# Kernel optimization log

Hardware: AMD Instinct MI355X
Metric: run time of the kernel (lower is better)

The kernel has to match this reference:

```python
import jax, jax.numpy as jnp
import numpy as np

N = 100000
E = 1600000
IN_CH, HID_CH, OUT_CH, HEADS = 128, 32, 64, 4
NEG_SLOPE = 0.2


def gat_conv(x, src, dst, W, att_src, att_dst, bias, concat):
    """PyG-style GATConv (inference; dropout off). src/dst include self-loops.
    x: [N, Fin], W: [Fin, H*C], att_*: [H, C], bias: [H*C] or [C]."""
    n = x.shape[0]
    H, C = att_src.shape
    h = (x @ W).reshape(n, H, C)                      # [N, H, C]
    a_s = jnp.sum(h * att_src, axis=-1)               # [N, H]
    a_d = jnp.sum(h * att_dst, axis=-1)               # [N, H]
    e = jax.nn.leaky_relu(a_s[src] + a_d[dst], NEG_SLOPE)   # [E, H]
    # segment softmax over incoming edges of each dst node
    e_max = jax.ops.segment_max(e, dst, num_segments=n)     # [N, H]
    e_exp = jnp.exp(e - e_max[dst])                          # [E, H]
    denom = jax.ops.segment_sum(e_exp, dst, num_segments=n) # [N, H]
    alpha = e_exp / (denom[dst] + 1e-16)                     # [E, H]
    msg = h[src] * alpha[:, :, None]                         # [E, H, C]
    out = jax.ops.segment_sum(msg, dst, num_segments=n)     # [N, H, C]
    out = out.reshape(n, H * C) if concat else out.mean(axis=1)
    return out + bias


def setup_inputs() -> dict:
    key = jax.random.key(0)
    ks = jax.random.split(key, 10)
    g = 1.0 / np.sqrt(IN_CH)
    g2 = 1.0 / np.sqrt(HID_CH * HEADS)
    return {
        "x": jax.random.normal(ks[0], (N, IN_CH), dtype=jnp.float32),
        "edge_index": jax.random.randint(ks[1], (2, E), 0, N, dtype=jnp.int64),
        "W1": jax.random.normal(ks[2], (IN_CH, HEADS * HID_CH), dtype=jnp.float32) * g,
        "att_src1": jax.random.normal(ks[3], (HEADS, HID_CH), dtype=jnp.float32) * g,
        "att_dst1": jax.random.normal(ks[4], (HEADS, HID_CH), dtype=jnp.float32) * g,
        "b1": jnp.zeros((HEADS * HID_CH,), dtype=jnp.float32),
        "W2": jax.random.normal(ks[5], (HEADS * HID_CH, OUT_CH), dtype=jnp.float32) * g2,
        "att_src2": jax.random.normal(ks[6], (1, OUT_CH), dtype=jnp.float32) * g2,
        "att_dst2": jax.random.normal(ks[7], (1, OUT_CH), dtype=jnp.float32) * g2,
        "b2": jnp.zeros((OUT_CH,), dtype=jnp.float32),
    }


def reference(x, edge_index, W1, att_src1, att_dst1, b1, W2, att_src2, att_dst2, b2):
    n = x.shape[0]
    # GATConv adds self-loops by default (fixed-size concat: jit friendly)
    loops = jnp.arange(n, dtype=edge_index.dtype)
    src = jnp.concatenate([edge_index[0], loops])
    dst = jnp.concatenate([edge_index[1], loops])
    h = gat_conv(x, src, dst, W1, att_src1, att_dst1, b1, concat=True)
    h = jax.nn.elu(h)
    return gat_conv(h, src, dst, W2, att_src2, att_dst2, b2, concat=False)
```

## Files before the change

kernel.cpp:

```cpp
#include <hip/hip_runtime.h>
#include <hip/hip_fp16.h>

#define NEG_SLOPE 0.2f
#define BKN 128
#define MAXNB 1024
#define GRP 256
#define LOG2E 1.44269504f

typedef _Float16 half_t;
typedef __attribute__((ext_vector_type(2))) _Float16 half2v;
typedef __attribute__((ext_vector_type(4))) _Float16 half4;
typedef __attribute__((ext_vector_type(8))) _Float16 half8;
typedef __attribute__((ext_vector_type(4))) float floatx4;

#if __has_builtin(__builtin_amdgcn_fdot2)
#define FDOT2(a, b, c) __builtin_amdgcn_fdot2((a), (b), (c), false)
#else
#define FDOT2(a, b, c) ((float)(a)[0] * (float)(b)[0] + (float)(a)[1] * (float)(b)[1] + (c))
#endif

template<int BN, int HEADS, bool INHALF>
__global__ __launch_bounds__(256) void gemm_mfma(
    const void* __restrict__ Xv, const half_t* __restrict__ Wt,
    const float* __restrict__ atts, const float* __restrict__ attd,
    half_t* __restrict__ H, float* __restrict__ As, float* __restrict__ Ad,
    int n)
{
    constexpr int K  = 128;
    constexpr int NT = BN / 16;
    constexpr int TPH = NT / HEADS;

    __shared__ half_t Wl[BN * K];
    __shared__ half_t Xl[64 * K];

    const int t = threadIdx.x;
    const int wave = t >> 6, lane = t & 63;
    const int quad = lane >> 4, c = lane & 15;

    float att_s[NT], att_d[NT];
    #pragma unroll
    for (int nt = 0; nt < NT; ++nt) {
        att_s[nt] = atts[nt * 16 + c] * LOG2E;
        att_d[nt] = attd[nt * 16 + c] * LOG2E;
    }

    for (int i = t; i < BN * 16; i += 256) {
        int row = i >> 4, cid = i & 15;
        half8 v = *(const half8*)(Wt + row * K + cid * 8);
        *(half8*)(Wl + row * K + ((cid ^ (row & 15)) << 3)) = v;
    }

    const int numTiles = (n + 63) / 64;
    for (int tile = blockIdx.x; tile < numTiles; tile += gridDim.x) {
        const int row0 = tile * 64;
        __syncthreads();
        for (int i = t; i < 1024; i += 256) {
            int m = i >> 4, cid = i & 15;
            int row = row0 + m;
            half8 h;
            #pragma unroll
            for (int z = 0; z < 8; ++z) h[z] = (half_t)0.f;
            if (row < n) {
                if constexpr (INHALF) {
                    h = *(const half8*)((const half_t*)Xv + (size_t)row * K + cid * 8);
                } else {
                    const float4* src = (const float4*)((const float*)Xv + (size_t)row * K + cid * 8);
                    float4 a = src[0], b = src[1];
                    h[0]=(half_t)a.x; h[1]=(half_t)a.y; h[2]=(half_t)a.z; h[3]=(half_t)a.w;
                    h[4]=(half_t)b.x; h[5]=(half_t)b.y; h[6]=(half_t)b.z; h[7]=(half_t)b.w;
                }
            }
            *(half8*)(Xl + m * K + ((cid ^ (m & 15)) << 3)) = h;
        }
        __syncthreads();

        floatx4 acc[NT];
        #pragma unroll
        for (int i = 0; i < NT; ++i) acc[i] = (floatx4)(0.f);

        #pragma unroll
        for (int kc = 0; kc < 4; ++kc) {
            int cid = kc * 4 + quad;
            half8 afrag = *(const half8*)(Xl + (wave * 16 + c) * K + ((cid ^ c) << 3));
            #pragma unroll
            for (int nt = 0; nt < NT; ++nt) {
                half8 bfrag = *(const half8*)(Wl + (nt * 16 + c) * K + ((cid ^ c) << 3));
                acc[nt] = __builtin_amdgcn_mfma_f32_16x16x32_f16(afrag, bfrag, acc[nt], 0, 0, 0);
            }
        }

        #pragma unroll
        for (int reg = 0; reg < 4; ++reg) {
            int row = row0 + wave * 16 + quad * 4 + reg;
            bool ok = row < n;
            if (ok) {
                #pragma unroll
                for (int nt = 0; nt < NT; ++nt)
                    H[(size_t)row * BN + nt * 16 + c] = (half_t)acc[nt][reg];
            }
            #pragma unroll
            for (int h = 0; h < HEADS; ++h) {
                float ps = 0.f, pd = 0.f;
                #pragma unroll
                for (int u = 0; u < TPH; ++u) {
                    int nt = h * TPH + u;
                    ps += acc[nt][reg] * att_s[nt];
                    pd += acc[nt][reg] * att_d[nt];
                }
                #pragma unroll
                for (int off = 1; off < 16; off <<= 1) {
                    ps += __shfl_xor(ps, off);
                    pd += __shfl_xor(pd, off);
                }
                if (ok && c == 0) {
                    As[(size_t)row * HEADS + h] = ps;
                    Ad[(size_t)row * HEADS + h] = pd;
                }
            }
        }
    }
}

__global__ __launch_bounds__(256) void ghist_wconv(
    const int* __restrict__ ei, int E, int Etot, int NB, int chunk,
    int* __restrict__ cnt,
    const float* __restrict__ W1, half_t* __restrict__ Wt1,
    const float* __restrict__ W2, half_t* __restrict__ Wt2)
{
    int iw = blockIdx.x * 256 + threadIdx.x;
    if (iw < 128 * 128) {
        int k = iw / 128, nn = iw % 128;
        Wt1[nn * 128 + k] = (half_t)W1[iw];
    } else if (iw < 128 * 128 + 128 * 64) {
        int jx = iw - 128 * 128;
        int k = jx / 64, nn = jx % 64;
        Wt2[nn * 128 + k] = (half_t)W2[jx];
    }

    __shared__ int h[MAXNB];
    int g = blockIdx.x;
    for (int i = threadIdx.x; i < NB; i += 256) h[i] = 0;
    __syncthreads();
    int lo = g * chunk, hi = min(Etot, lo + chunk);
    for (int e = lo + threadIdx.x; e < hi; e += 256) {
        int dst = (e < E) ? ei[E + e] : (e - E);
        atomicAdd(&h[dst >> 7], 1);
    }
    __syncthreads();
    for (int i = threadIdx.x; i < NB; i += 256) cnt[i * GRP + g] = h[i];
}

__global__ __launch_bounds__(256) void scan_blocks(
    int* __restrict__ data, int n, int* __restrict__ bsum)
{
    __shared__ int s[256];
    int t = threadIdx.x;
    int idx = blockIdx.x * 1024 + t * 4;
    int4 v = make_int4(0, 0, 0, 0);
    if (idx + 3 < n)      v = *(const int4*)(data + idx);
    else {
        if (idx     < n) v.x = data[idx];
        if (idx + 1 < n) v.y = data[idx+1];
        if (idx + 2 < n) v.z = data[idx+2];
        if (idx + 3 < n) v.w = data[idx+3];
    }
    int tsum = v.x + v.y + v.z + v.w;
    s[t] = tsum;
    __syncthreads();
    for (int off = 1; off < 256; off <<= 1) {
        int x = (t >= off) ? s[t - off] : 0;
        __syncthreads();
        s[t] += x;
        __syncthreads();
    }
    int excl = s[t] - tsum;
    if (t == 255) bsum[blockIdx.x] = s[255];
    if (idx     < n) data[idx]     = excl;
    if (idx + 1 < n) data[idx + 1] = excl + v.x;
    if (idx + 2 < n) data[idx + 2] = excl + v.x + v.y;
    if (idx + 3 < n) data[idx + 3] = excl + v.x + v.y + v.z;
}

__global__ __launch_bounds__(256) void scan_sums(int* __restrict__ bsum, int nb)
{
    __shared__ int s[256];
    int t = threadIdx.x;
    int v = (t < nb) ? bsum[t] : 0;
    s[t] = v;
    __syncthreads();
    for (int off = 1; off < 256; off <<= 1) {
        int x = (t >= off) ? s[t - off] : 0;
        __syncthreads();
        s[t] += x;
        __syncthreads();
    }
    if (t < nb) bsum[t] = s[t] - v;
}

__global__ __launch_bounds__(256) void pass1_gemm1(
    const int* __restrict__ ei, int E, int Etot, int NB, int chunk,
    const int* __restrict__ S, const int* __restrict__ bsum,
    unsigned* __restrict__ tmp,
    const float* __restrict__ X, const half_t* __restrict__ Wt,
    const float* __restrict__ atts, const float* __restrict__ attd,
    half_t* __restrict__ H, float* __restrict__ As, float* __restrict__ Ad,
    int n)
{
    constexpr int K = 128, BN = 128, NT = 8, HEADS = 4, TPH = 2;
    __shared__ half_t Wl[BN * K];
    __shared__ half_t Xl[64 * K];
    __shared__ int cur[MAXNB];

    const int t = threadIdx.x;

    if (blockIdx.x < GRP) {
        int g = blockIdx.x;
        for (int i = t; i < NB; i += 256) {
            int idx = i * GRP + g;
            cur[i] = S[idx] + bsum[idx >> 10];
        }
        __syncthreads();
        int lo = g * chunk, hi = min(Etot, lo + chunk);
        for (int e = lo + t; e < hi; e += 256) {
            int src, dst;
            if (e < E) { src = ei[e]; dst = ei[E + e]; }
            else       { src = dst = e - E; }
            int pos = atomicAdd(&cur[dst >> 7], 1);
            tmp[pos] = ((unsigned)src << 7) | (unsigned)(dst & (BKN - 1));
        }
        return;
    }

    const int wave = t >> 6, lane = t & 63;
    const int quad = lane >> 4, c = lane & 15;

    float att_s[NT], att_d[NT];
    #pragma unroll
    for (int nt = 0; nt < NT; ++nt) {
        att_s[nt] = atts[nt * 16 + c] * LOG2E;
        att_d[nt] = attd[nt * 16 + c] * LOG2E;
    }

    for (int i = t; i < BN * 16; i += 256) {
        int row = i >> 4, cid = i & 15;
        half8 v = *(const half8*)(Wt + row * K + cid * 8);
        *(half8*)(Wl + row * K + ((cid ^ (row & 15)) << 3)) = v;
    }

    const int numTiles = (n + 63) / 64;
    for (int tile = blockIdx.x - GRP; tile < numTiles; tile += gridDim.x - GRP) {
        const int row0 = tile * 64;
        __syncthreads();
        for (int i = t; i < 1024; i += 256) {
            int m = i >> 4, cid = i & 15;
            int row = row0 + m;
            half8 h;
            #pragma unroll
            for (int z = 0; z < 8; ++z) h[z] = (half_t)0.f;
            if (row < n) {
                const float4* src = (const float4*)(X + (size_t)row * K + cid * 8);
                float4 a = src[0], b = src[1];
                h[0]=(half_t)a.x; h[1]=(half_t)a.y; h[2]=(half_t)a.z; h[3]=(half_t)a.w;
                h[4]=(half_t)b.x; h[5]=(half_t)b.y; h[6]=(half_t)b.z; h[7]=(half_t)b.w;
            }
            *(half8*)(Xl + m * K + ((cid ^ (m & 15)) << 3)) = h;
        }
        __syncthreads();

        floatx4 acc[NT];
        #pragma unroll
        for (int i = 0; i < NT; ++i) acc[i] = (floatx4)(0.f);

        #pragma unroll
        for (int kc = 0; kc < 4; ++kc) {
            int cid = kc * 4 + quad;
            half8 afrag = *(const half8*)(Xl + (wave * 16 + c) * K + ((cid ^ c) << 3));
            #pragma unroll
            for (int nt = 0; nt < NT; ++nt) {
                half8 bfrag = *(const half8*)(Wl + (nt * 16 + c) * K + ((cid ^ c) << 3));
                acc[nt] = __builtin_amdgcn_mfma_f32_16x16x32_f16(afrag, bfrag, acc[nt], 0, 0, 0);
            }
        }

        #pragma unroll
        for (int reg = 0; reg < 4; ++reg) {
            int row = row0 + wave * 16 + quad * 4 + reg;
            bool ok = row < n;
            if (ok) {
                #pragma unroll
                for (int nt = 0; nt < NT; ++nt)
                    H[(size_t)row * BN + nt * 16 + c] = (half_t)acc[nt][reg];
            }
            #pragma unroll
            for (int h = 0; h < HEADS; ++h) {
                float ps = 0.f, pd = 0.f;
                #pragma unroll
                for (int u = 0; u < TPH; ++u) {
                    int nt = h * TPH + u;
                    ps += acc[nt][reg] * att_s[nt];
                    pd += acc[nt][reg] * att_d[nt];
                }
                #pragma unroll
                for (int off = 1; off < 16; off <<= 1) {
                    ps += __shfl_xor(ps, off);
                    pd += __shfl_xor(pd, off);
                }
                if (ok && c == 0) {
                    As[(size_t)row * HEADS + h] = ps;
                    Ad[(size_t)row * HEADS + h] = pd;
                }
            }
        }
    }
}

__global__ __launch_bounds__(256) void pass2_sort(
    const unsigned* __restrict__ tmp, const int* __restrict__ S,
    const int* __restrict__ bsum, int NB, int Etot,
    int* __restrict__ offs, int* __restrict__ esrc, int n)
{
    __shared__ int cnt[BKN];
    __shared__ int sc[BKN];
    __shared__ int cur[BKN];
    int bk = blockIdx.x;
    int t  = threadIdx.x;
    if (t < BKN) cnt[t] = 0;
    __syncthreads();
    int lo = S[bk * GRP] + bsum[(bk * GRP) >> 10];
    int hi = (bk + 1 < NB) ? (S[(bk + 1) * GRP] + bsum[((bk + 1) * GRP) >> 10]) : Etot;
    for (int i = lo + t; i < hi; i += 256)
        atomicAdd(&cnt[tmp[i] & (BKN - 1)], 1);
    __syncthreads();
    int v = (t < BKN) ? cnt[t] : 0;
    if (t < BKN) sc[t] = v;
    __syncthreads();
    for (int off = 1; off < BKN; off <<= 1) {
        int x = (t < BKN && t >= off) ? sc[t - off] : 0;
        __syncthreads();
        if (t < BKN) sc[t] += x;
        __syncthreads();
    }
    if (t < BKN) {
        int node = bk * BKN + t;
        if (node < n) offs[node] = lo + sc[t];
        cur[t] = lo + sc[t] - v;
    }
    __syncthreads();
    for (int i = lo + t; i < hi; i += 256) {
        unsigned w = tmp[i];
        int p = atomicAdd(&cur[w & (BKN - 1)], 1);
        esrc[p] = (int)(w >> 7);
    }
}

__global__ __launch_bounds__(256) void agg1(
    const int* __restrict__ offs, const int* __restrict__ esrc,
    const half8* __restrict__ H8, const float* __restrict__ As,
    const float* __restrict__ Ad, const float* __restrict__ bias,
    half_t* __restrict__ X2h, int n)
{
    int v    = (blockIdx.x * 256 + threadIdx.x) >> 6;
    int lane = threadIdx.x & 63;
    if (v >= n) return;
    int q    = lane >> 4;
    int li   = lane & 15;
    int head = li >> 2;
    int end = offs[v];
    int beg = v ? offs[v - 1] : 0;
    float adv = Ad[(size_t)v * 4 + head];
    half2v one; one[0] = (half_t)1.f; one[1] = (half_t)1.f;
    float a[8];
    #pragma unroll
    for (int f = 0; f < 8; ++f) a[f] = 0.f;
    float den = 0.f;
    int j = beg + q;
    for (; j + 12 < end; j += 16) {
        int s0 = esrc[j], s1 = esrc[j + 4], s2 = esrc[j + 8], s3 = esrc[j + 12];
        float e0 = As[(unsigned)(s0 * 4 + head)] + adv;
        float e1 = As[(unsigned)(s1 * 4 + head)] + adv;
        float e2 = As[(unsigned)(s2 * 4 + head)] + adv;
        float e3 = As[(unsigned)(s3 * 4 + head)] + adv;
        half8 q0 = H8[(unsigned)(s0 * 16 + li)];
        half8 q1 = H8[(unsigned)(s1 * 16 + li)];
        half8 q2 = H8[(unsigned)(s2 * 16 + li)];
        half8 q3 = H8[(unsigned)(s3 * 16 + li)];
        float w0 = __builtin_amdgcn_exp2f(fmaxf(e0, NEG_SLOPE * e0));
        float w1 = __builtin_amdgcn_exp2f(fmaxf(e1, NEG_SLOPE * e1));
        float w2 = __builtin_amdgcn_exp2f(fmaxf(e2, NEG_SLOPE * e2));
        float w3 = __builtin_amdgcn_exp2f(fmaxf(e3, NEG_SLOPE * e3));
        half2v wp01; wp01[0] = (half_t)w0; wp01[1] = (half_t)w1;
        half2v wp23; wp23[0] = (half_t)w2; wp23[1] = (half_t)w3;
        #pragma unroll
        for (int f = 0; f < 8; ++f) {
            half2v p01; p01[0] = q0[f]; p01[1] = q1[f];
            half2v p23; p23[0] = q2[f]; p23[1] = q3[f];
            a[f] = FDOT2(p01, wp01, a[f]);
            a[f] = FDOT2(p23, wp23, a[f]);
        }
        den = FDOT2(wp01, one, den);
        den = FDOT2(wp23, one, den);
    }
    for (; j + 4 < end; j += 8) {
        int s0 = esrc[j], s1 = esrc[j + 4];
        float e0 = As[(unsigned)(s0 * 4 + head)] + adv;
        float e1 = As[(unsigned)(s1 * 4 + head)] + adv;
        half8 q0 = H8[(unsigned)(s0 * 16 + li)];
        half8 q1 = H8[(unsigned)(s1 * 16 + li)];
        float w0 = __builtin_amdgcn_exp2f(fmaxf(e0, NEG_SLOPE * e0));
        float w1 = __builtin_amdgcn_exp2f(fmaxf(e1, NEG_SLOPE * e1));
        half2v wp; wp[0] = (half_t)w0; wp[1] = (half_t)w1;
        #pragma unroll
        for (int f = 0; f < 8; ++f) {
            half2v p; p[0] = q0[f]; p[1] = q1[f];
            a[f] = FDOT2(p, wp, a[f]);
        }
        den = FDOT2(wp, one, den);
    }
    for (; j < end; j += 4) {
        int s = esrc[j];
        float e = As[(unsigned)(s * 4 + head)] + adv;
        half8 q0 = H8[(unsigned)(s * 16 + li)];
        float w = __builtin_amdgcn_exp2f(fmaxf(e, NEG_SLOPE * e));
        #pragma unroll
        for (int f = 0; f < 8; ++f) a[f] += w * (float)q0[f];
        den += w;
    }
    #pragma unroll
    for (int f = 0; f < 8; ++f) {
        a[f] += __shfl_xor(a[f], 16);
        a[f] += __shfl_xor(a[f], 32);
    }
    den += __shfl_xor(den, 16);
    den += __shfl_xor(den, 32);
    if (q == 0) {
        float inv = 1.f / (den + 1e-16f);
        float4 b0 = ((const float4*)bias)[2 * li];
        float4 b1 = ((const float4*)bias)[2 * li + 1];
        float o[8];
        o[0] = a[0] * inv + b0.x; o[1] = a[1] * inv + b0.y;
        o[2] = a[2] * inv + b0.z; o[3] = a[3] * inv + b0.w;
        o[4] = a[4] * inv + b1.x; o[5] = a[5] * inv + b1.y;
        o[6] = a[6] * inv + b1.z; o[7] = a[7] * inv + b1.w;
        half8 h;
        #pragma unroll
        for (int f = 0; f < 8; ++f) {
            float e = o[f] > 0.f ? o[f] : __expf(o[f]) - 1.f;
            h[f] = (half_t)e;
        }
        *(half8*)(X2h + (size_t)v * 128 + li * 8) = h;
    }
}

__global__ __launch_bounds__(256) void agg2(
    const int* __restrict__ offs, const int* __restrict__ esrc,
    const half8* __restrict__ H8, const float* __restrict__ As,
    const float* __restrict__ Ad, const float* __restrict__ bias,
    float* __restrict__ out, int n)
{
    int v    = (blockIdx.x * 256 + threadIdx.x) >> 6;
    int lane = threadIdx.x & 63;
    if (v >= n) return;
    int g  = lane >> 3;
    int li = lane & 7;
    int end = offs[v];
    int beg = v ? offs[v - 1] : 0;
    float adv = Ad[v];
    half2v one; one[0] = (half_t)1.f; one[1] = (half_t)1.f;
    float a[8];
    #pragma unroll
    for (int f = 0; f < 8; ++f) a[f] = 0.f;
    float den = 0.f;
    int j = beg + g;
    for (; j + 24 < end; j += 32) {
        int s0 = esrc[j], s1 = esrc[j + 8], s2 = esrc[j + 16], s3 = esrc[j + 24];
        float e0 = As[s0] + adv;
        float e1 = As[s1] + adv;
        float e2 = As[s2] + adv;
        float e3 = As[s3] + adv;
        half8 q0 = H8[(unsigned)(s0 * 8 + li)];
        half8 q1 = H8[(unsigned)(s1 * 8 + li)];
        half8 q2 = H8[(unsigned)(s2 * 8 + li)];
        half8 q3 = H8[(unsigned)(s3 * 8 + li)];
        float w0 = __builtin_amdgcn_exp2f(fmaxf(e0, NEG_SLOPE * e0));
        float w1 = __builtin_amdgcn_exp2f(fmaxf(e1, NEG_SLOPE * e1));
        float w2 = __builtin_amdgcn_exp2f(fmaxf(e2, NEG_SLOPE * e2));
        float w3 = __builtin_amdgcn_exp2f(fmaxf(e3, NEG_SLOPE * e3));
        half2v wp01; wp01[0] = (half_t)w0; wp01[1] = (half_t)w1;
        half2v wp23; wp23[0] = (half_t)w2; wp23[1] = (half_t)w3;
        #pragma unroll
        for (int f = 0; f < 8; ++f) {
            half2v p01; p01[0] = q0[f]; p01[1] = q1[f];
            half2v p23; p23[0] = q2[f]; p23[1] = q3[f];
            a[f] = FDOT2(p01, wp01, a[f]);
            a[f] = FDOT2(p23, wp23, a[f]);
        }
        den = FDOT2(wp01, one, den);
        den = FDOT2(wp23, one, den);
    }
    for (; j + 8 < end; j += 16) {
        int s0 = esrc[j], s1 = esrc[j + 8];
        float e0 = As[s0] + adv;
        float e1 = As[s1] + adv;
        half8 q0 = H8[(unsigned)(s0 * 8 + li)];
        half8 q1 = H8[(unsigned)(s1 * 8 + li)];
        float w0 = __builtin_amdgcn_exp2f(fmaxf(e0, NEG_SLOPE * e0));
        float w1 = __builtin_amdgcn_exp2f(fmaxf(e1, NEG_SLOPE * e1));
        half2v wp; wp[0] = (half_t)w0; wp[1] = (half_t)w1;
        #pragma unroll
        for (int f = 0; f < 8; ++f) {
            half2v p; p[0] = q0[f]; p[1] = q1[f];
            a[f] = FDOT2(p, wp, a[f]);
        }
        den = FDOT2(wp, one, den);
    }
    for (; j < end; j += 8) {
        int s = esrc[j];
        float e = As[s] + adv;
        half8 q0 = H8[(unsigned)(s * 8 + li)];
        float w = __builtin_amdgcn_exp2f(fmaxf(e, NEG_SLOPE * e));
        #pragma unroll
        for (int f = 0; f < 8; ++f) a[f] += w * (float)q0[f];
        den += w;
    }
    #pragma unroll
    for (int f = 0; f < 8; ++f) {
        a[f] += __shfl_xor(a[f], 8);
        a[f] += __shfl_xor(a[f], 16);
        a[f] += __shfl_xor(a[f], 32);
    }
    den += __shfl_xor(den, 8);
    den += __shfl_xor(den, 16);
    den += __shfl_xor(den, 32);
    if (lane < 8) {
        float inv = 1.f / (den + 1e-16f);
        float4 b0 = ((const float4*)bias)[2 * li];
        float4 b1 = ((const float4*)bias)[2 * li + 1];
        float4* o4 = (float4*)(out + (size_t)v * 64);
        o4[2 * li]     = make_float4(a[0] * inv + b0.x, a[1] * inv + b0.y,
                                     a[2] * inv + b0.z, a[3] * inv + b0.w);
        o4[2 * li + 1] = make_float4(a[4] * inv + b1.x, a[5] * inv + b1.y,
                                     a[6] * inv + b1.z, a[7] * inv + b1.w);
    }
}

extern "C" void kernel_launch(void* const* d_in, const int* in_sizes, int n_in,
                              void* d_out, int out_size, void* d_ws, size_t ws_size,
                              hipStream_t stream)
{
    (void)n_in; (void)out_size; (void)ws_size;
    const float* x   = (const float*)d_in[0];
    const int*   ei  = (const int*)  d_in[1];
    const float* W1  = (const float*)d_in[2];
    const float* as1 = (const float*)d_in[3];
    const float* ad1 = (const float*)d_in[4];
    const float* b1  = (const float*)d_in[5];
    const float* W2  = (const float*)d_in[6];
    const float* as2 = (const float*)d_in[7];
    const float* ad2 = (const float*)d_in[8];
    const float* b2  = (const float*)d_in[9];
    float* out = (float*)d_out;

    const int n    = in_sizes[0] / 128;
    const int E    = in_sizes[1] / 2;
    const int Etot = E + n;
    const int NB   = (n + BKN - 1) / BKN;
    const int chunk = (Etot + GRP - 1) / GRP;

    char* p = (char*)d_ws;
    half_t* Hh  = (half_t*)p; p += (size_t)n * 128 * sizeof(half_t);
    half_t* X2h = (half_t*)p; p += (size_t)n * 128 * sizeof(half_t);
    float* As1 = (float*)p;   p += (size_t)n * 4 * sizeof(float);
    float* Ad1 = (float*)p;   p += (size_t)n * 4 * sizeof(float);
    int* offs  = (int*)p;     p += (size_t)n * sizeof(int);
    int* esrc  = (int*)p;     p += (size_t)Etot * sizeof(int);
    unsigned* tmp = (unsigned*)p; p += (size_t)Etot * sizeof(unsigned);
    int* cnt   = (int*)p;     p += (size_t)NB * GRP * sizeof(int);
    int* bsum  = (int*)p;     p += 1024;
    half_t* Wt1 = (half_t*)p; p += 128 * 128 * sizeof(half_t);
    half_t* Wt2 = (half_t*)p; p += 64 * 128 * sizeof(half_t);

    const int scan_n  = NB * GRP;
    const int scan_nb = (scan_n + 1023) / 1024;

    const int gtiles = (n + 63) / 64;

    ghist_wconv<<<GRP, 256, 0, stream>>>(ei, E, Etot, NB, chunk, cnt, W1, Wt1, W2, Wt2);
    scan_blocks<<<scan_nb, 256, 0, stream>>>(cnt, scan_n, bsum);
    scan_sums<<<1, 256, 0, stream>>>(bsum, scan_nb);
    pass1_gemm1<<<GRP + gtiles, 256, 0, stream>>>(ei, E, Etot, NB, chunk, cnt, bsum, tmp,
                                                  x, Wt1, as1, ad1, Hh, As1, Ad1, n);
    pass2_sort<<<NB, 256, 0, stream>>>(tmp, cnt, bsum, NB, Etot, offs, esrc, n);

    agg1<<<(n * 64 + 255) / 256, 256, 0, stream>>>(offs, esrc, (const half8*)Hh, As1, Ad1, b1, X2h, n);

    gemm_mfma<64, 1, true><<<gtiles, 256, 0, stream>>>(X2h, Wt2, as2, ad2, Hh, As1, Ad1, n);
    agg2<<<(n * 64 + 255) / 256, 256, 0, stream>>>(offs, esrc, (const half8*)Hh, As1, Ad1, b2, out, n);
}
```

Measured before the change: 305.0 us.

## Drop scan_sums kernel and compute per-node degrees in histogram pass

The block-sum scan is folded into pass1 and pass2 so each block redundantly scans the small bsum array, which removes one kernel launch. Per-node degrees are accumulated with global atomics during the histogram pass. That lets pass2 skip its first counting sweep over tmp. The cost is a memset, 1.7M global atomics on deg, and a redundant 256-wide scan in every block.

```diff
diff --git a/kernel.cpp b/kernel.cpp
--- a/kernel.cpp
+++ b/kernel.cpp
@@ -123,7 +123,7 @@
 
 __global__ __launch_bounds__(256) void ghist_wconv(
     const int* __restrict__ ei, int E, int Etot, int NB, int chunk,
-    int* __restrict__ cnt,
+    int* __restrict__ cnt, int* __restrict__ deg,
     const float* __restrict__ W1, half_t* __restrict__ Wt1,
     const float* __restrict__ W2, half_t* __restrict__ Wt2)
 {
@@ -145,6 +145,7 @@
     for (int e = lo + threadIdx.x; e < hi; e += 256) {
         int dst = (e < E) ? ei[E + e] : (e - E);
         atomicAdd(&h[dst >> 7], 1);
+        atomicAdd(&deg[dst], 1);
     }
     __syncthreads();
     for (int i = threadIdx.x; i < NB; i += 256) cnt[i * GRP + g] = h[i];
@@ -181,24 +182,8 @@
     if (idx + 3 < n) data[idx + 3] = excl + v.x + v.y + v.z;
 }
 
-__global__ __launch_bounds__(256) void scan_sums(int* __restrict__ bsum, int nb)
-{
-    __shared__ int s[256];
-    int t = threadIdx.x;
-    int v = (t < nb) ? bsum[t] : 0;
-    s[t] = v;
-    __syncthreads();
-    for (int off = 1; off < 256; off <<= 1) {
-        int x = (t >= off) ? s[t - off] : 0;
-        __syncthreads();
-        s[t] += x;
-        __syncthreads();
-    }
-    if (t < nb) bsum[t] = s[t] - v;
-}
-
 __global__ __launch_bounds__(256) void pass1_gemm1(
-    const int* __restrict__ ei, int E, int Etot, int NB, int chunk,
+    const int* __restrict__ ei, int E, int Etot, int NB, int chunk, int nbC,
     const int* __restrict__ S, const int* __restrict__ bsum,
     unsigned* __restrict__ tmp,
     const float* __restrict__ X, const half_t* __restrict__ Wt,
@@ -214,10 +199,23 @@
     const int t = threadIdx.x;
 
     if (blockIdx.x < GRP) {
+        int* bs  = (int*)Wl;
+        int* bse = (int*)Wl + 256;
         int g = blockIdx.x;
+        int val = (t < nbC) ? bsum[t] : 0;
+        bs[t] = val;
+        __syncthreads();
+        for (int off = 1; off < 256; off <<= 1) {
+            int x = (t >= off) ? bs[t - off] : 0;
+            __syncthreads();
+            bs[t] += x;
+            __syncthreads();
+        }
+        bse[t] = bs[t] - val;
+        __syncthreads();
         for (int i = t; i < NB; i += 256) {
             int idx = i * GRP + g;
-            cur[i] = S[idx] + bsum[idx >> 10];
+            cur[i] = S[idx] + bse[idx >> 10];
         }
         __syncthreads();
         int lo = g * chunk, hi = min(Etot, lo + chunk);
@@ -314,25 +312,37 @@
     }
 }
 
-__global__ __launch_bounds__(256) void pass2_sort(
+__global__ __launch_bounds__(256) void pass2_lite(
     const unsigned* __restrict__ tmp, const int* __restrict__ S,
-    const int* __restrict__ bsum, int NB, int Etot,
+    const int* __restrict__ bsum, const int* __restrict__ deg,
+    int NB, int Etot, int nbC,
     int* __restrict__ offs, int* __restrict__ esrc, int n)
 {
-    __shared__ int cnt[BKN];
     __shared__ int sc[BKN];
     __shared__ int cur[BKN];
+    __shared__ int bs[256];
+    __shared__ int bse[256];
     int bk = blockIdx.x;
     int t  = threadIdx.x;
-    if (t < BKN) cnt[t] = 0;
+
+    int val = (t < nbC) ? bsum[t] : 0;
+    bs[t] = val;
     __syncthreads();
-    int lo = S[bk * GRP] + bsum[(bk * GRP) >> 10];
-    int hi = (bk + 1 < NB) ? (S[(bk + 1) * GRP] + bsum[((bk + 1) * GRP) >> 10]) : Etot;
-    for (int i = lo + t; i < hi; i += 256)
-        atomicAdd(&cnt[tmp[i] & (BKN - 1)], 1);
+    for (int off = 1; off < 256; off <<= 1) {
+        int x = (t >= off) ? bs[t - off] : 0;
+        __syncthreads();
+        bs[t] += x;
+        __syncthreads();
+    }
+    bse[t] = bs[t] - val;
     __syncthreads();
-    int v = (t < BKN) ? cnt[t] : 0;
-    if (t < BKN) sc[t] = v;
+
+    int lo = S[bk * GRP] + bse[(bk * GRP) >> 10];
+    int hi = (bk + 1 < NB) ? (S[(bk + 1) * GRP] + bse[((bk + 1) * GRP) >> 10]) : Etot;
+
+    int node = bk * BKN + t;
+    int d = (t < BKN && node < n) ? deg[node] : 0;
+    if (t < BKN) sc[t] = d;
     __syncthreads();
     for (int off = 1; off < BKN; off <<= 1) {
         int x = (t < BKN && t >= off) ? sc[t - off] : 0;
@@ -341,9 +351,8 @@
         __syncthreads();
     }
     if (t < BKN) {
-        int node = bk * BKN + t;
         if (node < n) offs[node] = lo + sc[t];
-        cur[t] = lo + sc[t] - v;
+        cur[t] = lo + sc[t] - d;
     }
     __syncthreads();
     for (int i = lo + t; i < hi; i += 256) {
@@ -571,6 +580,7 @@
     half_t* X2h = (half_t*)p; p += (size_t)n * 128 * sizeof(half_t);
     float* As1 = (float*)p;   p += (size_t)n * 4 * sizeof(float);
     float* Ad1 = (float*)p;   p += (size_t)n * 4 * sizeof(float);
+    int* deg   = (int*)p;     p += (size_t)n * sizeof(int);
     int* offs  = (int*)p;     p += (size_t)n * sizeof(int);
     int* esrc  = (int*)p;     p += (size_t)Etot * sizeof(int);
     unsigned* tmp = (unsigned*)p; p += (size_t)Etot * sizeof(unsigned);
@@ -584,12 +594,12 @@
 
     const int gtiles = (n + 63) / 64;
 
-    ghist_wconv<<<GRP, 256, 0, stream>>>(ei, E, Etot, NB, chunk, cnt, W1, Wt1, W2, Wt2);
+    hipMemsetAsync(deg, 0, (size_t)n * sizeof(int), stream);
+    ghist_wconv<<<GRP, 256, 0, stream>>>(ei, E, Etot, NB, chunk, cnt, deg, W1, Wt1, W2, Wt2);
     scan_blocks<<<scan_nb, 256, 0, stream>>>(cnt, scan_n, bsum);
-    scan_sums<<<1, 256, 0, stream>>>(bsum, scan_nb);
-    pass1_gemm1<<<GRP + gtiles, 256, 0, stream>>>(ei, E, Etot, NB, chunk, cnt, bsum, tmp,
+    pass1_gemm1<<<GRP + gtiles, 256, 0, stream>>>(ei, E, Etot, NB, chunk, scan_nb, cnt, bsum, tmp,
                                                   x, Wt1, as1, ad1, Hh, As1, Ad1, n);
-    pass2_sort<<<NB, 256, 0, stream>>>(tmp, cnt, bsum, NB, Etot, offs, esrc, n);
+    pass2_lite<<<NB, 256, 0, stream>>>(tmp, cnt, bsum, deg, NB, Etot, scan_nb, offs, esrc, n);
 
     agg1<<<(n * 64 + 255) / 256, 256, 0, stream>>>(offs, esrc, (const half8*)Hh, As1, Ad1, b1, X2h, n);
 
```

New measurement: 354.7 us. 1.16x slower.
